# Kernel optimization log

Hardware: AMD Instinct MI355X
Metric: run time of the kernel (lower is better)

Reference implementation:

```python
import jax, jax.numpy as jnp
import numpy as np

B, D, C = 2048, 1024, 8192


def setup_inputs() -> dict:
    key = jax.random.key(0)
    k1, k2, k3 = jax.random.split(key, 3)
    x = jax.random.normal(k1, (B, D), dtype=jnp.float32)
    y = jax.random.randint(k2, (B,), 0, C)
    centroids = jax.random.normal(k3, (C, D), dtype=jnp.float32)
    return {"x": x, "y": y, "centroids": centroids}


def reference(x, y, centroids):
    x2 = jnp.sum(x * x, axis=-1, keepdims=True)          # (B, 1)
    c2 = jnp.sum(centroids * centroids, axis=-1)          # (C,)
    logits = -(x2 + c2[None, :] - 2.0 * (x @ centroids.T))  # (B, C)
    decisions = jnp.argmax(logits, axis=1)                # nearest centroid
    score = jnp.mean((decisions == y).astype(jnp.float32))
    # CrossEntropyLoss(distances, y)
    logp = jax.nn.log_softmax(logits, axis=-1)
    loss = -jnp.mean(jnp.take_along_axis(logp, y[:, None], axis=1))
    return loss, score
```

## Files before the change

kernel.cpp:

```cpp
#include <hip/hip_runtime.h>
#include <cstdint>

#define MDIM 2048
#define KDIM 1024
#define CDIM 8192
#define BM 256
#define BN 256
#define BK 32
#define NT (KDIM / BK)
#define NCHUNK (CDIM / 64)
#define CVT_BLOCKS 1280

typedef __attribute__((ext_vector_type(8))) __bf16 bf16x8;
typedef __attribute__((ext_vector_type(4))) float f32x4;
typedef __attribute__((ext_vector_type(8))) unsigned short ushort8;

__device__ __forceinline__ unsigned short f2bf(float f) {
  unsigned u = __float_as_uint(f);
  u += 0x7fffu + ((u >> 16) & 1u);
  return (unsigned short)(u >> 16);
}

__device__ __forceinline__ void async_ld16(const void* g, void* l) {
  __builtin_amdgcn_global_load_lds(
      (__attribute__((address_space(1))) void*)(g),
      (__attribute__((address_space(3))) void*)(l),
      16, 0, 0);
}

__global__ __launch_bounds__(256) void convert_all(const float* __restrict__ x,
                                                   const float* __restrict__ cent,
                                                   unsigned short* __restrict__ xb,
                                                   unsigned short* __restrict__ cb,
                                                   float* __restrict__ c2) {
  const int t = threadIdx.x;
  const int wv = t >> 6, lane = t & 63;
  const int rsel = wv >> 1;
  const int half = wv & 1;
  const int eidx = half * 64 + lane;
  __shared__ float red[4];
  for (int p = blockIdx.x; p < (MDIM + CDIM) / 2; p += CVT_BLOCKS) {
    const int row = p * 2 + rsel;
    const bool isc = row >= MDIM;
    const float* srcrow = isc ? (cent + (size_t)(row - MDIM) * KDIM)
                              : (x + (size_t)row * KDIM);
    const float4* src = (const float4*)srcrow + eidx * 2;
    const float4 v0 = src[0], v1 = src[1];
    ushort8 o;
    o[0] = f2bf(v0.x); o[1] = f2bf(v0.y); o[2] = f2bf(v0.z); o[3] = f2bf(v0.w);
    o[4] = f2bf(v1.x); o[5] = f2bf(v1.y); o[6] = f2bf(v1.z); o[7] = f2bf(v1.w);
    if (!isc) {
      ((ushort8*)(xb + (size_t)row * KDIM))[eidx] = o;
    } else {
      ((ushort8*)(cb + (size_t)(row - MDIM) * KDIM))[eidx] = o;
      float pq = v0.x * v0.x + v0.y * v0.y + v0.z * v0.z + v0.w * v0.w
               + v1.x * v1.x + v1.y * v1.y + v1.z * v1.z + v1.w * v1.w;
      for (int d = 32; d; d >>= 1) pq += __shfl_down(pq, d, 64);
      if (lane == 0) red[wv] = pq;
    }
    __syncthreads();
    if (isc && half == 0 && lane == 0)
      c2[row - MDIM] = red[wv] + red[wv + 1];
    __syncthreads();
  }
}

__global__ __launch_bounds__(512, 2) void gemm_reduce(
    const unsigned short* __restrict__ Ab, const unsigned short* __restrict__ Bb,
    const float* __restrict__ c2,
    float* __restrict__ pm, float* __restrict__ pl, int* __restrict__ pidx) {
  __shared__ __align__(16) char lds[4 * 32768];

  const int tid = threadIdx.x;
  const int wave = tid >> 6, lane = tid & 63;
  const int wm = wave >> 2, wn = wave & 3;
  const int quad = lane >> 4, c16 = lane & 15;

  const int id = blockIdx.y * gridDim.x + blockIdx.x;
  const int lid = (id & 7) * 32 + (id >> 3);
  const int bm = lid >> 5, bn = lid & 31;
  const int bmBase = bm * BM, bnBase = bn * BN;

  const int r1 = tid >> 2, c1 = (tid & 3) ^ ((r1 >> 1) & 3);
  const int r2 = (tid + 512) >> 2, c2s = (tid & 3) ^ ((r2 >> 1) & 3);
  const char* Ag1 = (const char*)(Ab + (size_t)(bmBase + r1) * KDIM + c1 * 8);
  const char* Ag2 = (const char*)(Ab + (size_t)(bmBase + r2) * KDIM + c2s * 8);
  const char* Bg1 = (const char*)(Bb + (size_t)(bnBase + r1) * KDIM + c1 * 8);
  const char* Bg2 = (const char*)(Bb + (size_t)(bnBase + r2) * KDIM + c2s * 8);
  const int wbyte = wave * 1024;

  int aoff[8], boff[4];
#pragma unroll
  for (int mt = 0; mt < 8; ++mt) {
    const int row = wm * 128 + mt * 16 + c16;
    aoff[mt] = row * 64 + ((quad ^ ((row >> 1) & 3)) * 16);
  }
#pragma unroll
  for (int nt = 0; nt < 4; ++nt) {
    const int col = wn * 64 + nt * 16 + c16;
    boff[nt] = col * 64 + ((quad ^ ((col >> 1) & 3)) * 16);
  }

  f32x4 acc[8][4] = {};

#define STAGE(T)                                          \
  {                                                       \
    const int _ko = (T) * (BK * 2);                       \
    char* _sb = &lds[((T) & 3) * 32768];                  \
    async_ld16(Ag1 + _ko, _sb + wbyte);                   \
    async_ld16(Ag2 + _ko, _sb + 8192 + wbyte);            \
    async_ld16(Bg1 + _ko, _sb + 16384 + wbyte);           \
    async_ld16(Bg2 + _ko, _sb + 24576 + wbyte);           \
  }

  STAGE(0); STAGE(1); STAGE(2);

#pragma unroll 1
  for (int t = 0; t < NT; ++t) {
    if (t < NT - 2)       asm volatile("s_waitcnt vmcnt(8)" ::: "memory");
    else if (t == NT - 2) asm volatile("s_waitcnt vmcnt(4)" ::: "memory");
    else                  asm volatile("s_waitcnt vmcnt(0)" ::: "memory");
    __builtin_amdgcn_s_barrier();
    __builtin_amdgcn_sched_barrier(0);

    const char* sb = &lds[(t & 3) * 32768];
    bf16x8 a[8], b[4];
#pragma unroll
    for (int mt = 0; mt < 8; ++mt) a[mt] = *(const bf16x8*)(sb + aoff[mt]);
#pragma unroll
    for (int nt = 0; nt < 4; ++nt) b[nt] = *(const bf16x8*)(sb + 16384 + boff[nt]);

    if (t < NT - 3) STAGE(t + 3);

    asm volatile("s_waitcnt lgkmcnt(0)" ::: "memory");
    __builtin_amdgcn_sched_barrier(0);
    __builtin_amdgcn_s_setprio(1);
#pragma unroll
    for (int mt = 0; mt < 8; ++mt)
#pragma unroll
      for (int nt = 0; nt < 4; ++nt)
        acc[mt][nt] = __builtin_amdgcn_mfma_f32_16x16x32_bf16(a[mt], b[nt], acc[mt][nt], 0, 0, 0);
    __builtin_amdgcn_s_setprio(0);
  }
#undef STAGE

  const int colbase = bnBase + wn * 64;
  float c2v[4];
#pragma unroll
  for (int nt = 0; nt < 4; ++nt) c2v[nt] = c2[colbase + nt * 16 + c16];

  const int chunk = bn * 4 + wn;
#pragma unroll
  for (int mt = 0; mt < 8; ++mt) {
#pragma unroll
    for (int r = 0; r < 4; ++r) {
      float sv[4];
#pragma unroll
      for (int nt = 0; nt < 4; ++nt) sv[nt] = 2.0f * acc[mt][nt][r] - c2v[nt];
      float m = sv[0];
      int idx = colbase + c16;
#pragma unroll
      for (int nt = 1; nt < 4; ++nt) {
        if (sv[nt] > m) { m = sv[nt]; idx = colbase + nt * 16 + c16; }
      }
      float l = 0.f;
#pragma unroll
      for (int nt = 0; nt < 4; ++nt) l += __expf(sv[nt] - m);
      for (int d = 1; d < 16; d <<= 1) {
        float om = __shfl_xor(m, d, 64);
        float ol = __shfl_xor(l, d, 64);
        int oi = __shfl_xor(idx, d, 64);
        float M = fmaxf(m, om);
        l = l * __expf(m - M) + ol * __expf(om - M);
        idx = (om > m || (om == m && oi < idx)) ? oi : idx;
        m = M;
      }
      if (c16 == 0) {
        const int row = bmBase + wm * 128 + mt * 16 + quad * 4 + r;
        pm[(size_t)row * NCHUNK + chunk] = m;
        pl[(size_t)row * NCHUNK + chunk] = l;
        pidx[(size_t)row * NCHUNK + chunk] = idx;
      }
    }
  }
}

__global__ __launch_bounds__(64) void combine_kernel(
    const float* __restrict__ pm, const float* __restrict__ pl,
    const int* __restrict__ pidx, const float* __restrict__ x,
    const float* __restrict__ cent, const float* __restrict__ c2,
    const int* __restrict__ y,
    float* __restrict__ loss_part, float* __restrict__ corr_part) {
  const int row = blockIdx.x, t = threadIdx.x;
  const int yc = y[row];
  const size_t base = (size_t)row * NCHUNK;

  const float m0 = pm[base + t],      l0 = pl[base + t];
  const float m1 = pm[base + t + 64], l1 = pl[base + t + 64];
  const int   i0 = pidx[base + t],    i1 = pidx[base + t + 64];
  float m = fmaxf(m0, m1);
  float l = l0 * __expf(m0 - m) + l1 * __expf(m1 - m);
  int idx = (m1 > m0) ? i1 : i0;

  const float4* xa = (const float4*)(x + (size_t)row * KDIM) + t * 4;
  const float4* ca = (const float4*)(cent + (size_t)yc * KDIM) + t * 4;
  float dot = 0.f;
#pragma unroll
  for (int j = 0; j < 4; ++j) {
    const float4 a = xa[j], b = ca[j];
    dot += a.x * b.x + a.y * b.y + a.z * b.z + a.w * b.w;
  }

  for (int d = 1; d < 64; d <<= 1) {
    const float om = __shfl_xor(m, d, 64);
    const float ol = __shfl_xor(l, d, 64);
    const int oi = __shfl_xor(idx, d, 64);
    const float od = __shfl_xor(dot, d, 64);
    const float M = fmaxf(m, om);
    l = l * __expf(m - M) + ol * __expf(om - M);
    idx = (om > m || (om == m && oi < idx)) ? oi : idx;
    m = M;
    dot += od;
  }
  if (t == 0) {
    const float sy = 2.0f * dot - c2[yc];
    loss_part[row] = __logf(l) + m - sy;
    corr_part[row] = (idx == yc) ? 1.f : 0.f;
  }
}

__global__ __launch_bounds__(256) void finalize(const float* __restrict__ loss_part,
                                                const float* __restrict__ corr_part,
                                                float* __restrict__ out) {
  const int t = threadIdx.x;
  float s0 = 0.f, s1 = 0.f;
  for (int i = t; i < MDIM; i += 256) { s0 += loss_part[i]; s1 += corr_part[i]; }
  for (int d = 32; d; d >>= 1) {
    s0 += __shfl_down(s0, d, 64);
    s1 += __shfl_down(s1, d, 64);
  }
  __shared__ float r0[4], r1[4];
  if ((t & 63) == 0) { r0[t >> 6] = s0; r1[t >> 6] = s1; }
  __syncthreads();
  if (t == 0) {
    out[0] = (r0[0] + r0[1] + r0[2] + r0[3]) * (1.0f / MDIM);
    out[1] = (r1[0] + r1[1] + r1[2] + r1[3]) * (1.0f / MDIM);
  }
}

extern "C" void kernel_launch(void* const* d_in, const int* in_sizes, int n_in,
                              void* d_out, int out_size, void* d_ws, size_t ws_size,
                              hipStream_t stream) {
  const float* x = (const float*)d_in[0];
  const int* y = (const int*)d_in[1];
  const float* cent = (const float*)d_in[2];
  float* out = (float*)d_out;

  char* ws = (char*)d_ws;
  const size_t OFF_XB = 0;
  const size_t OFF_CB = OFF_XB + (size_t)MDIM * KDIM * 2;
  const size_t OFF_C2 = OFF_CB + (size_t)CDIM * KDIM * 2;
  const size_t OFF_PM = OFF_C2 + (size_t)CDIM * 4;
  const size_t OFF_PL = OFF_PM + (size_t)NCHUNK * MDIM * 4;
  const size_t OFF_PI = OFF_PL + (size_t)NCHUNK * MDIM * 4;
  const size_t OFF_LP = OFF_PI + (size_t)NCHUNK * MDIM * 4;
  const size_t OFF_CP = OFF_LP + (size_t)MDIM * 4;
  const size_t NEED = OFF_CP + (size_t)MDIM * 4;
  if (ws_size < NEED) return;

  unsigned short* xb = (unsigned short*)(ws + OFF_XB);
  unsigned short* cb = (unsigned short*)(ws + OFF_CB);
  float* c2 = (float*)(ws + OFF_C2);
  float* pm = (float*)(ws + OFF_PM);
  float* pl = (float*)(ws + OFF_PL);
  int* pidx = (int*)(ws + OFF_PI);
  float* loss_part = (float*)(ws + OFF_LP);
  float* corr_part = (float*)(ws + OFF_CP);

  convert_all<<<CVT_BLOCKS, 256, 0, stream>>>(x, cent, xb, cb, c2);
  gemm_reduce<<<dim3(CDIM / BN, MDIM / BM), 512, 0, stream>>>(xb, cb, c2, pm, pl, pidx);
  combine_kernel<<<MDIM, 64, 0, stream>>>(pm, pl, pidx, x, cent, c2, y, loss_part, corr_part);
  finalize<<<1, 256, 0, stream>>>(loss_part, corr_part, out);
}
```

Before: 138.0 us.

## Switch GEMM to 32x32x16 MFMA tiles with matching LDS reads and epilogue

Replaces the 16x16x32 bf16 MFMA tiling (8x4 tiles per wave) with 32x32x16 MFMA (4x2 tiles per wave, two k-halves per 32-wide K step). LDS fragment loads, swizzled offsets and the fused softmax/argmax epilogue are rewritten for the 32x32 accumulator layout, including a wider 32-lane shuffle reduction. Larger MFMA tiles cut the instruction count and LDS reads per FLOP. In exchange, each row now needs a 5-step shuffle reduction instead of 4.

```diff
diff --git a/kernel.cpp b/kernel.cpp
--- a/kernel.cpp
+++ b/kernel.cpp
@@ -13,6 +13,7 @@
 
 typedef __attribute__((ext_vector_type(8))) __bf16 bf16x8;
 typedef __attribute__((ext_vector_type(4))) float f32x4;
+typedef __attribute__((ext_vector_type(16))) float f32x16;
 typedef __attribute__((ext_vector_type(8))) unsigned short ushort8;
 
 __device__ __forceinline__ unsigned short f2bf(float f) {
@@ -74,7 +75,7 @@
   const int tid = threadIdx.x;
   const int wave = tid >> 6, lane = tid & 63;
   const int wm = wave >> 2, wn = wave & 3;
-  const int quad = lane >> 4, c16 = lane & 15;
+  const int l31 = lane & 31, hi = lane >> 5;
 
   const int id = blockIdx.y * gridDim.x + blockIdx.x;
   const int lid = (id & 7) * 32 + (id >> 3);
@@ -89,19 +90,25 @@
   const char* Bg2 = (const char*)(Bb + (size_t)(bnBase + r2) * KDIM + c2s * 8);
   const int wbyte = wave * 1024;
 
-  int aoff[8], boff[4];
-#pragma unroll
-  for (int mt = 0; mt < 8; ++mt) {
-    const int row = wm * 128 + mt * 16 + c16;
-    aoff[mt] = row * 64 + ((quad ^ ((row >> 1) & 3)) * 16);
-  }
-#pragma unroll
-  for (int nt = 0; nt < 4; ++nt) {
-    const int col = wn * 64 + nt * 16 + c16;
-    boff[nt] = col * 64 + ((quad ^ ((col >> 1) & 3)) * 16);
-  }
-
-  f32x4 acc[8][4] = {};
+  int aoff[4][2], boff[2][2];
+#pragma unroll
+  for (int mt = 0; mt < 4; ++mt) {
+    const int row = wm * 128 + mt * 32 + l31;
+    const int s = (row >> 1) & 3;
+#pragma unroll
+    for (int kh = 0; kh < 2; ++kh)
+      aoff[mt][kh] = row * 64 + (((kh * 2 + hi) ^ s) * 16);
+  }
+#pragma unroll
+  for (int nt = 0; nt < 2; ++nt) {
+    const int col = wn * 64 + nt * 32 + l31;
+    const int s = (col >> 1) & 3;
+#pragma unroll
+    for (int kh = 0; kh < 2; ++kh)
+      boff[nt][kh] = 16384 + col * 64 + (((kh * 2 + hi) ^ s) * 16);
+  }
+
+  f32x16 acc[4][2] = {};
 
 #define STAGE(T)                                          \
   {                                                       \
@@ -124,11 +131,15 @@
     __builtin_amdgcn_sched_barrier(0);
 
     const char* sb = &lds[(t & 3) * 32768];
-    bf16x8 a[8], b[4];
-#pragma unroll
-    for (int mt = 0; mt < 8; ++mt) a[mt] = *(const bf16x8*)(sb + aoff[mt]);
-#pragma unroll
-    for (int nt = 0; nt < 4; ++nt) b[nt] = *(const bf16x8*)(sb + 16384 + boff[nt]);
+    bf16x8 a[4][2], b[2][2];
+#pragma unroll
+    for (int mt = 0; mt < 4; ++mt)
+#pragma unroll
+      for (int kh = 0; kh < 2; ++kh) a[mt][kh] = *(const bf16x8*)(sb + aoff[mt][kh]);
+#pragma unroll
+    for (int nt = 0; nt < 2; ++nt)
+#pragma unroll
+      for (int kh = 0; kh < 2; ++kh) b[nt][kh] = *(const bf16x8*)(sb + boff[nt][kh]);
 
     if (t < NT - 3) STAGE(t + 3);
 
@@ -136,37 +147,33 @@
     __builtin_amdgcn_sched_barrier(0);
     __builtin_amdgcn_s_setprio(1);
 #pragma unroll
-    for (int mt = 0; mt < 8; ++mt)
-#pragma unroll
-      for (int nt = 0; nt < 4; ++nt)
-        acc[mt][nt] = __builtin_amdgcn_mfma_f32_16x16x32_bf16(a[mt], b[nt], acc[mt][nt], 0, 0, 0);
+    for (int kh = 0; kh < 2; ++kh)
+#pragma unroll
+      for (int mt = 0; mt < 4; ++mt)
+#pragma unroll
+        for (int nt = 0; nt < 2; ++nt)
+          acc[mt][nt] = __builtin_amdgcn_mfma_f32_32x32x16_bf16(a[mt][kh], b[nt][kh], acc[mt][nt], 0, 0, 0);
     __builtin_amdgcn_s_setprio(0);
   }
 #undef STAGE
 
   const int colbase = bnBase + wn * 64;
-  float c2v[4];
-#pragma unroll
-  for (int nt = 0; nt < 4; ++nt) c2v[nt] = c2[colbase + nt * 16 + c16];
-
+  const float c2v0 = c2[colbase + l31];
+  const float c2v1 = c2[colbase + 32 + l31];
   const int chunk = bn * 4 + wn;
-#pragma unroll
-  for (int mt = 0; mt < 8; ++mt) {
-#pragma unroll
-    for (int r = 0; r < 4; ++r) {
-      float sv[4];
-#pragma unroll
-      for (int nt = 0; nt < 4; ++nt) sv[nt] = 2.0f * acc[mt][nt][r] - c2v[nt];
-      float m = sv[0];
-      int idx = colbase + c16;
-#pragma unroll
-      for (int nt = 1; nt < 4; ++nt) {
-        if (sv[nt] > m) { m = sv[nt]; idx = colbase + nt * 16 + c16; }
-      }
-      float l = 0.f;
-#pragma unroll
-      for (int nt = 0; nt < 4; ++nt) l += __expf(sv[nt] - m);
-      for (int d = 1; d < 16; d <<= 1) {
+
+#pragma unroll
+  for (int mt = 0; mt < 4; ++mt) {
+#pragma unroll
+    for (int reg = 0; reg < 16; ++reg) {
+      const float sv0 = 2.0f * acc[mt][0][reg] - c2v0;
+      const float sv1 = 2.0f * acc[mt][1][reg] - c2v1;
+      float m;
+      int idx;
+      if (sv1 > sv0) { m = sv1; idx = colbase + 32 + l31; }
+      else           { m = sv0; idx = colbase + l31; }
+      float l = __expf(sv0 - m) + __expf(sv1 - m);
+      for (int d = 1; d < 32; d <<= 1) {
         float om = __shfl_xor(m, d, 64);
         float ol = __shfl_xor(l, d, 64);
         int oi = __shfl_xor(idx, d, 64);
@@ -175,8 +182,8 @@
         idx = (om > m || (om == m && oi < idx)) ? oi : idx;
         m = M;
       }
-      if (c16 == 0) {
-        const int row = bmBase + wm * 128 + mt * 16 + quad * 4 + r;
+      if (l31 == 0) {
+        const int row = bmBase + wm * 128 + mt * 32 + (reg & 3) + 8 * (reg >> 2) + 4 * hi;
         pm[(size_t)row * NCHUNK + chunk] = m;
         pl[(size_t)row * NCHUNK + chunk] = l;
         pidx[(size_t)row * NCHUNK + chunk] = idx;
```

New measurement: 160.7 us. +16.4%, slower.
